# Optimization experiments

Hardware: AMD Instinct MI355X
Metric: run time of the kernel (lower is better)

Reference implementation:

```python
import jax, jax.numpy as jnp
import numpy as np


def setup_inputs() -> dict:
    key = jax.random.key(0)
    ks = jax.random.split(key, 6)
    B, S, D, E, F = 4, 2048, 1024, 8, 2048
    return {
        "hidden_states": jax.random.normal(ks[0], (B, S, D), dtype=jnp.float32),
        "attention_mask": jnp.ones((B, S), dtype=jnp.int32),
        "router_w": jax.random.normal(ks[1], (D, E), dtype=jnp.float32) * (D ** -0.5),
        "w1": jax.random.normal(ks[2], (E, D, F), dtype=jnp.float32) * (D ** -0.5),
        "b1": jnp.zeros((E, F), dtype=jnp.float32),
        "w2": jax.random.normal(ks[3], (E, F, D), dtype=jnp.float32) * (F ** -0.5),
        "b2": jnp.zeros((E, D), dtype=jnp.float32),
        "top_k": 2,
    }


def reference(hidden_states, attention_mask, router_w, w1, b1, w2, b2, top_k):
    B, S, D = hidden_states.shape
    E = router_w.shape[1]
    # Router: logits -> softmax -> top-k -> renormalize weights (weights / weight_sum)
    logits = jnp.einsum('bsd,de->bse', hidden_states, router_w)          # [B,S,E]
    probs = jax.nn.softmax(logits, axis=-1)
    top_w, top_i = jax.lax.top_k(probs, top_k)                           # [B,S,k]
    top_w = top_w / jnp.sum(top_w, axis=-1, keepdims=True)
    # Dense combine weights: [B,S,E], zero except the selected experts
    combine = jnp.sum(jax.nn.one_hot(top_i, E, dtype=hidden_states.dtype)
                      * top_w[..., None], axis=-2)                       # [B,S,E]
    # All-expert MLP (ReLU), then weighted combine
    h = jax.nn.relu(jnp.einsum('bsd,edf->ebsf', hidden_states, w1)
                    + b1[:, None, None, :])                              # [E,B,S,F]
    y = jnp.einsum('ebsf,efd->ebsd', h, w2) + b2[:, None, None, :]       # [E,B,S,D]
    out = jnp.einsum('bse,ebsd->bsd', combine, y)                        # [B,S,D]
    # Masked tokens remain zero (as in the original Python loop)
    out = jnp.where((attention_mask != 0)[..., None], out, 0.0)
    return out
```

## Files before the change

kernel.cpp:

```cpp
#include <hip/hip_runtime.h>

typedef __attribute__((ext_vector_type(8))) short short8;
typedef __attribute__((ext_vector_type(4))) float floatx4;

static constexpr int D = 1024;
static constexpr int F = 2048;
static constexpr int E = 8;
static constexpr int TOK = 4 * 2048;
static constexpr int RTOT = 2 * TOK;
static constexpr int MT = 24;
static constexpr int RBLK = 512;

__device__ __forceinline__ unsigned short f2bf(float f) {
  unsigned int u = __float_as_uint(f);
  unsigned int r = (u + 0x7fffu + ((u >> 16) & 1u)) >> 16;
  return (unsigned short)r;
}

__device__ __forceinline__ void glds16(const unsigned short* g, unsigned short* l) {
  __builtin_amdgcn_global_load_lds(
      (const __attribute__((address_space(1))) void*)g,
      (__attribute__((address_space(3))) void*)l, 16, 0, 0);
}

__global__ __launch_bounds__(256) void router_kernel(
    const float* __restrict__ hs, const int* __restrict__ mask,
    const float* __restrict__ rw, int2* __restrict__ te, float2* __restrict__ tw,
    int* __restrict__ blkcnt, unsigned short* __restrict__ Xbf) {
  __shared__ float rwT[E][D];
  __shared__ int cnt[16];
  int tid = threadIdx.x;
  if (tid < 16) cnt[tid] = 0;
#pragma unroll
  for (int q = 0; q < 4; ++q) {
    int i = tid * 4 + q;
    float4 a = *(const float4*)(rw + (size_t)i * E);
    float4 b = *(const float4*)(rw + (size_t)i * E + 4);
    rwT[0][i] = a.x; rwT[1][i] = a.y; rwT[2][i] = a.z; rwT[3][i] = a.w;
    rwT[4][i] = b.x; rwT[5][i] = b.y; rwT[6][i] = b.z; rwT[7][i] = b.w;
  }
  __syncthreads();

  int lane = tid & 63, wid = tid >> 6;
  int tok0 = blockIdx.x * 16 + wid * 4;
#pragma unroll 1
  for (int tt = 0; tt < 4; ++tt) {
    int t = tok0 + tt;
    const float* x = hs + (size_t)t * D;
    float acc[E];
#pragma unroll
    for (int e = 0; e < E; ++e) acc[e] = 0.f;
#pragma unroll
    for (int j = 0; j < 4; ++j) {
      int i0 = j * 256 + lane * 4;
      float4 xv = *(const float4*)(x + i0);
      union { unsigned short u[4]; uint2 q; } p;
      p.u[0] = f2bf(xv.x); p.u[1] = f2bf(xv.y);
      p.u[2] = f2bf(xv.z); p.u[3] = f2bf(xv.w);
      *(uint2*)(Xbf + (size_t)t * D + i0) = p.q;
#pragma unroll
      for (int e = 0; e < E; ++e) {
        float4 rv = *(const float4*)&rwT[e][i0];
        acc[e] += xv.x * rv.x + xv.y * rv.y + xv.z * rv.z + xv.w * rv.w;
      }
    }
#pragma unroll
    for (int off = 32; off > 0; off >>= 1) {
#pragma unroll
      for (int e = 0; e < E; ++e) acc[e] += __shfl_xor(acc[e], off, 64);
    }
    if (lane == 0) {
      int i1 = 0;
#pragma unroll
      for (int e = 1; e < E; ++e) if (acc[e] > acc[i1]) i1 = e;
      int i2 = (i1 == 0) ? 1 : 0;
#pragma unroll
      for (int e = 0; e < E; ++e) if (e != i1 && acc[e] > acc[i2]) i2 = e;
      float mx = fmaxf(acc[i1], acc[i2]);
      float e1 = expf(acc[i1] - mx), e2 = expf(acc[i2] - mx);
      float s = e1 + e2;
      float m = (mask[t] != 0) ? 1.f : 0.f;
      te[t] = make_int2(i1, i2);
      tw[t] = make_float2(e1 / s * m, e2 / s * m);
      atomicAdd(&cnt[i1], 1);
      atomicAdd(&cnt[8 + i2], 1);
    }
  }
  __syncthreads();
  if (tid < 16) blkcnt[blockIdx.x * 16 + tid] = cnt[tid];
}

__global__ __launch_bounds__(256) void prefix_kernel(const int* __restrict__ blkcnt,
                                                     int* __restrict__ meta) {
  __shared__ int part[256];
  int tid = threadIdx.x;
  int c = tid & 15, g = tid >> 4;
  int s = 0;
  for (int b = g; b < RBLK; b += 16) s += blkcnt[b * 16 + c];
  part[tid] = s;
  __syncthreads();
  if (tid < 16) {
    int tot = 0;
#pragma unroll
    for (int g2 = 0; g2 < 16; ++g2) tot += part[g2 * 16 + tid];
    meta[tid] = tot;
  }
  __syncthreads();
  if (tid == 0) {
    int run = 0;
    for (int e = 0; e < E; ++e) {
      meta[16 + e] = run;
      meta[24 + e] = run + meta[e];
      run += meta[e] + meta[8 + e];
    }
  }
}

__global__ __launch_bounds__(256) void scatter_kernel(
    const int2* __restrict__ te, const float2* __restrict__ tw,
    int* __restrict__ meta, int* __restrict__ LIST, float* __restrict__ WTS,
    int* __restrict__ slotp, int* __restrict__ slots) {
  int t = blockIdx.x * 256 + threadIdx.x;
  int lane = threadIdx.x & 63;
  int2 e = te[t];
  float2 w = tw[t];
#pragma unroll
  for (int ex = 0; ex < E; ++ex) {
    unsigned long long m1 = __ballot(e.x == ex);
    if (m1) {
      int leader = __ffsll((long long)m1) - 1;
      int base = 0;
      if (lane == leader) base = atomicAdd(&meta[32 + ex], (int)__popcll(m1));
      base = __shfl(base, leader, 64);
      if (e.x == ex) {
        int pos = (int)__popcll(m1 & ((1ull << lane) - 1ull));
        int s1 = meta[16 + ex] + base + pos;
        LIST[s1] = t; WTS[s1] = w.x; slotp[t] = s1;
      }
    }
    unsigned long long m2 = __ballot(e.y == ex);
    if (m2) {
      int leader = __ffsll((long long)m2) - 1;
      int base = 0;
      if (lane == leader) base = atomicAdd(&meta[40 + ex], (int)__popcll(m2));
      base = __shfl(base, leader, 64);
      if (e.y == ex) {
        int pos = (int)__popcll(m2 & ((1ull << lane) - 1ull));
        int s2 = meta[24 + ex] + base + pos;
        LIST[s2] = t; WTS[s2] = w.y; slots[t] = s2;
      }
    }
  }
}

__global__ __launch_bounds__(256) void cvtw_kernel(const float* __restrict__ src,
                                                   unsigned short* __restrict__ dst,
                                                   int K, int N) {
  int e = blockIdx.x, k0 = blockIdx.y * 64, n0 = blockIdx.z * 64;
  src += (size_t)e * K * N;
  dst += (size_t)e * K * N;
  __shared__ float t[64][65];
  int tid = threadIdx.x;
  int tr = tid >> 4, tc = (tid & 15) * 4;
#pragma unroll
  for (int i = 0; i < 4; ++i) {
    int k = tr + i * 16;
    float4 v = *(const float4*)(src + (size_t)(k0 + k) * N + n0 + tc);
    t[k][tc] = v.x; t[k][tc + 1] = v.y; t[k][tc + 2] = v.z; t[k][tc + 3] = v.w;
  }
  __syncthreads();
  int n = tid >> 2, kk = (tid & 3) * 16;
  union { unsigned short u[16]; uint4 q[2]; } p;
#pragma unroll
  for (int j = 0; j < 16; ++j) p.u[j] = f2bf(t[kk + j][n]);
  uint4* o = (uint4*)(dst + (size_t)(n0 + n) * K + k0 + kk);
  o[0] = p.q[0]; o[1] = p.q[1];
}

template <int EPI, int K, int N>
__global__ __launch_bounds__(256) void moe_gemm(
    const unsigned short* __restrict__ Abase,
    const unsigned short* __restrict__ Wt,
    const float* __restrict__ bias,
    const int* __restrict__ LIST, const float* __restrict__ WTS,
    const int* __restrict__ meta,
    unsigned short* __restrict__ HcOut,
    float* __restrict__ YcOut,
    float* __restrict__ out) {
  constexpr int NT = N / 128;
  int bx = blockIdx.x;
  int e = bx & 7;
  int t = bx >> 3;
  int n0 = (t % NT) * 128;
  int m = t / NT;
  int cnt = meta[e] + meta[8 + e];
  int mrow = m * 128;
  if (mrow >= cnt) return;
  int rowStart = meta[16 + e] + mrow;
  int rowsLeft = cnt - mrow; if (rowsLeft > 128) rowsLeft = 128;

  __shared__ unsigned short As[128 * 32];
  __shared__ unsigned short Bs[128 * 32];
  int tid = threadIdx.x;
  int lane = tid & 63, wid = tid >> 6;
  int wm = (wid >> 1) * 64, wn = (wid & 1) * 64;
  int lr = lane & 15, lq = lane >> 4;

  int sr = tid >> 2;
  int sc = (tid & 3) ^ (sr & 3);
  const unsigned short* gA[2];
  const unsigned short* gB[2];
  const unsigned short* wb = Wt + (size_t)e * N * K;
#pragma unroll
  for (int q = 0; q < 2; ++q) {
    int r = q * 64 + sr;
    int ar = r < rowsLeft ? r : rowsLeft - 1;
    int arow = (EPI == 1) ? LIST[rowStart + ar] : (rowStart + ar);
    gA[q] = Abase + (size_t)arow * K + sc * 8;
    gB[q] = wb + (size_t)(n0 + r) * K + sc * 8;
  }

  floatx4 acc[4][4];
#pragma unroll
  for (int i = 0; i < 4; ++i)
#pragma unroll
    for (int j = 0; j < 4; ++j) acc[i][j] = (floatx4){0.f, 0.f, 0.f, 0.f};

  for (int k0 = 0; k0 < K; k0 += 32) {
    __syncthreads();
    glds16(gA[0] + k0, &As[tid * 8]);
    glds16(gA[1] + k0, &As[2048 + tid * 8]);
    glds16(gB[0] + k0, &Bs[tid * 8]);
    glds16(gB[1] + k0, &Bs[2048 + tid * 8]);
    __syncthreads();
    short8 af[4], bfr[4];
#pragma unroll
    for (int i = 0; i < 4; ++i) {
      int row = wm + i * 16 + lr;
      int ch = lq ^ (row & 3);
      af[i] = *(const short8*)&As[row * 32 + ch * 8];
    }
#pragma unroll
    for (int j = 0; j < 4; ++j) {
      int row = wn + j * 16 + lr;
      int ch = lq ^ (row & 3);
      bfr[j] = *(const short8*)&Bs[row * 32 + ch * 8];
    }
#pragma unroll
    for (int i = 0; i < 4; ++i)
#pragma unroll
      for (int j = 0; j < 4; ++j)
        acc[i][j] = __builtin_amdgcn_mfma_f32_16x16x32_bf16(af[i], bfr[j], acc[i][j], 0, 0, 0);
  }

  const float* be = bias + (size_t)e * N;
  if (EPI == 1) {
#pragma unroll
    for (int i = 0; i < 4; ++i) {
#pragma unroll
      for (int j = 0; j < 4; ++j) {
        int col = n0 + wn + j * 16 + lr;
        float bv = be[col];
#pragma unroll
        for (int r = 0; r < 4; ++r) {
          int row = wm + i * 16 + lq * 4 + r;
          if (row < rowsLeft) {
            float v = fmaxf(acc[i][j][r] + bv, 0.f);
            HcOut[(size_t)(rowStart + row) * N + col] = f2bf(v);
          }
        }
      }
    }
  } else {
#pragma unroll
    for (int i = 0; i < 4; ++i) {
      int tokr[4]; float wtr[4]; bool val[4];
#pragma unroll
      for (int r = 0; r < 4; ++r) {
        int row = wm + i * 16 + lq * 4 + r;
        val[r] = row < rowsLeft;
        int gi = rowStart + (val[r] ? row : 0);
        if (EPI == 0) tokr[r] = LIST[gi];
        wtr[r] = WTS[gi];
      }
#pragma unroll
      for (int j = 0; j < 4; ++j) {
        int col = n0 + wn + j * 16 + lr;
        float bv = be[col];
#pragma unroll
        for (int r = 0; r < 4; ++r) {
          if (val[r]) {
            float v = wtr[r] * (acc[i][j][r] + bv);
            if (EPI == 0) {
              atomicAdd(&out[(size_t)tokr[r] * N + col], v);
            } else {
              int row = wm + i * 16 + lq * 4 + r;
              YcOut[(size_t)(rowStart + row) * N + col] = v;
            }
          }
        }
      }
    }
  }
}

__global__ __launch_bounds__(256) void combine_kernel(
    const float* __restrict__ Yc, const int* __restrict__ slotp,
    const int* __restrict__ slots, float* __restrict__ out) {
  int t = blockIdx.x;
  int d4 = threadIdx.x * 4;
  int s1 = slotp[t], s2 = slots[t];
  float4 a = *(const float4*)(Yc + (size_t)s1 * D + d4);
  float4 b = *(const float4*)(Yc + (size_t)s2 * D + d4);
  float4 o;
  o.x = a.x + b.x; o.y = a.y + b.y; o.z = a.z + b.z; o.w = a.w + b.w;
  *(float4*)(out + (size_t)t * D + d4) = o;
}

extern "C" void kernel_launch(void* const* d_in, const int* in_sizes, int n_in,
                              void* d_out, int out_size, void* d_ws, size_t ws_size,
                              hipStream_t stream) {
  (void)in_sizes; (void)n_in;
  const float* hs   = (const float*)d_in[0];
  const int*   mask = (const int*)d_in[1];
  const float* rw   = (const float*)d_in[2];
  const float* w1   = (const float*)d_in[3];
  const float* b1   = (const float*)d_in[4];
  const float* w2   = (const float*)d_in[5];
  const float* b2   = (const float*)d_in[6];
  float* out = (float*)d_out;

  char* ws = (char*)d_ws;
  int* meta  = (int*)ws;
  int2* te   = (int2*)(ws + 1024);
  float2* tw = (float2*)(ws + 1024 + (size_t)TOK * 8);
  int* LIST  = (int*)(ws + 1024 + (size_t)TOK * 16);
  float* WTS = (float*)(ws + 1024 + (size_t)TOK * 16 + (size_t)RTOT * 4);
  int* slotp = (int*)(ws + 1024 + (size_t)TOK * 16 + (size_t)RTOT * 8);
  int* slots = (int*)(ws + 1024 + (size_t)TOK * 16 + (size_t)RTOT * 8 + (size_t)TOK * 4);
  int* blkcnt = (int*)(ws + (512 << 10));
  unsigned short* Xbf = (unsigned short*)(ws + (1 << 20));
  unsigned short* Hc  = (unsigned short*)(ws + (1 << 20) + (size_t)TOK * D * 2);
  unsigned short* Wt  = (unsigned short*)(ws + (1 << 20) + (size_t)TOK * D * 2 +
                                          (size_t)RTOT * F * 2);
  size_t yc_off = (size_t)(1 << 20) + (size_t)TOK * D * 2 + (size_t)RTOT * F * 2 +
                  (size_t)E * (size_t)D * F * 2;
  float* Yc = (float*)(ws + yc_off);
  bool wide = ws_size >= yc_off + (size_t)RTOT * D * 4;

  hipMemsetAsync(meta, 0, 256, stream);
  if (!wide) hipMemsetAsync(out, 0, (size_t)out_size * sizeof(float), stream);
  router_kernel<<<RBLK, 256, 0, stream>>>(hs, mask, rw, te, tw, blkcnt, Xbf);
  prefix_kernel<<<1, 256, 0, stream>>>(blkcnt, meta);
  scatter_kernel<<<TOK / 256, 256, 0, stream>>>(te, tw, meta, LIST, WTS, slotp, slots);
  cvtw_kernel<<<dim3(E, D / 64, F / 64), 256, 0, stream>>>(w1, Wt, D, F);
  moe_gemm<1, D, F><<<E * MT * (F / 128), 256, 0, stream>>>(
      Xbf, Wt, b1, LIST, WTS, meta, Hc, nullptr, nullptr);
  cvtw_kernel<<<dim3(E, F / 64, D / 64), 256, 0, stream>>>(w2, Wt, F, D);
  if (wide) {
    moe_gemm<2, F, D><<<E * MT * (D / 128), 256, 0, stream>>>(
        Hc, Wt, b2, LIST, WTS, meta, nullptr, Yc, nullptr);
    combine_kernel<<<TOK, 256, 0, stream>>>(Yc, slotp, slots, out);
  } else {
    moe_gemm<0, F, D><<<E * MT * (D / 128), 256, 0, stream>>>(
        Hc, Wt, b2, LIST, WTS, meta, nullptr, nullptr, out);
  }
}
```

Measured before the change: 452.9 us.

## Double-buffer LDS tiles in expert GEMM and drop XOR swizzle

Splits the shared-memory A/B tiles into two ping-pong buffers so the global-to-LDS loads for the next K slice are issued before the MFMAs on the current slice. This halves the number of barriers per K step and aims to hide load latency behind compute. It also removes the XOR chunk swizzle on both the store and read paths. That simplifies addressing but may add LDS bank conflicts on the fragment reads. The barrier's wait on outstanding loads may limit how much overlap is actually achieved.

```diff
diff --git a/kernel.cpp b/kernel.cpp
--- a/kernel.cpp
+++ b/kernel.cpp
@@ -199,15 +199,17 @@
   int rowStart = meta[16 + e] + mrow;
   int rowsLeft = cnt - mrow; if (rowsLeft > 128) rowsLeft = 128;
 
-  __shared__ unsigned short As[128 * 32];
-  __shared__ unsigned short Bs[128 * 32];
+  __shared__ unsigned short As0[128 * 32];
+  __shared__ unsigned short Bs0[128 * 32];
+  __shared__ unsigned short As1[128 * 32];
+  __shared__ unsigned short Bs1[128 * 32];
   int tid = threadIdx.x;
   int lane = tid & 63, wid = tid >> 6;
   int wm = (wid >> 1) * 64, wn = (wid & 1) * 64;
   int lr = lane & 15, lq = lane >> 4;
 
   int sr = tid >> 2;
-  int sc = (tid & 3) ^ (sr & 3);
+  int sc = tid & 3;
   const unsigned short* gA[2];
   const unsigned short* gB[2];
   const unsigned short* wb = Wt + (size_t)e * N * K;
@@ -226,32 +228,43 @@
 #pragma unroll
     for (int j = 0; j < 4; ++j) acc[i][j] = (floatx4){0.f, 0.f, 0.f, 0.f};
 
-  for (int k0 = 0; k0 < K; k0 += 32) {
+#define STAGE(kk, A_, B_)                         \
+  do {                                            \
+    glds16(gA[0] + (kk), &A_[tid * 8]);           \
+    glds16(gA[1] + (kk), &A_[2048 + tid * 8]);    \
+    glds16(gB[0] + (kk), &B_[tid * 8]);           \
+    glds16(gB[1] + (kk), &B_[2048 + tid * 8]);    \
+  } while (0)
+
+#define COMPUTE(A_, B_)                                                          \
+  do {                                                                           \
+    short8 af[4], bfr[4];                                                        \
+    _Pragma("unroll")                                                            \
+    for (int i = 0; i < 4; ++i)                                                  \
+      af[i] = *(const short8*)&A_[(wm + i * 16 + lr) * 32 + lq * 8];             \
+    _Pragma("unroll")                                                            \
+    for (int j = 0; j < 4; ++j)                                                  \
+      bfr[j] = *(const short8*)&B_[(wn + j * 16 + lr) * 32 + lq * 8];            \
+    _Pragma("unroll")                                                            \
+    for (int i = 0; i < 4; ++i)                                                  \
+      _Pragma("unroll")                                                          \
+      for (int j = 0; j < 4; ++j)                                                \
+        acc[i][j] = __builtin_amdgcn_mfma_f32_16x16x32_bf16(af[i], bfr[j],       \
+                                                            acc[i][j], 0, 0, 0); \
+  } while (0)
+
+  STAGE(0, As0, Bs0);
+  __syncthreads();
+  for (int k0 = 0; k0 < K; k0 += 64) {
+    STAGE(k0 + 32, As1, Bs1);
+    COMPUTE(As0, Bs0);
     __syncthreads();
-    glds16(gA[0] + k0, &As[tid * 8]);
-    glds16(gA[1] + k0, &As[2048 + tid * 8]);
-    glds16(gB[0] + k0, &Bs[tid * 8]);
-    glds16(gB[1] + k0, &Bs[2048 + tid * 8]);
+    if (k0 + 64 < K) STAGE(k0 + 64, As0, Bs0);
+    COMPUTE(As1, Bs1);
     __syncthreads();
-    short8 af[4], bfr[4];
-#pragma unroll
-    for (int i = 0; i < 4; ++i) {
-      int row = wm + i * 16 + lr;
-      int ch = lq ^ (row & 3);
-      af[i] = *(const short8*)&As[row * 32 + ch * 8];
-    }
-#pragma unroll
-    for (int j = 0; j < 4; ++j) {
-      int row = wn + j * 16 + lr;
-      int ch = lq ^ (row & 3);
-      bfr[j] = *(const short8*)&Bs[row * 32 + ch * 8];
-    }
-#pragma unroll
-    for (int i = 0; i < 4; ++i)
-#pragma unroll
-      for (int j = 0; j < 4; ++j)
-        acc[i][j] = __builtin_amdgcn_mfma_f32_16x16x32_bf16(af[i], bfr[j], acc[i][j], 0, 0, 0);
-  }
+  }
+#undef STAGE
+#undef COMPUTE
 
   const float* be = bias + (size_t)e * N;
   if (EPI == 1) {
```

Result: no change. 452.8 us (-0.0%).
